# Kernel optimization log

Measured on AMD Instinct MI355X. Metric: run time of the kernel, lower is better.

## Reference

```python
import jax, jax.numpy as jnp
import numpy as np
from jax import lax

B, IN_N, OUT_N, SEQ, HID = 8, 16, 16, 256, 64
NUM_C = 64 + 3  # grid_size + spline_order
EPS_LN = 1e-5


def setup_inputs():
    key = jax.random.key(0)
    k = jax.random.split(key, 8)
    f32 = jnp.float32
    return {
        "x_in": jax.random.normal(k[0], (B, IN_N, SEQ, HID), f32),
        "proj_x_prev": jax.random.normal(k[1], (B, IN_N, SEQ, HID), f32),
        "spline_weights": jax.random.normal(k[2], (IN_N, OUT_N, NUM_C), f32) * 0.1,
        "base_scales": 0.6 + 0.1 * jax.random.normal(k[3], (IN_N, OUT_N), f32),
        "tau": jax.random.normal(k[4], (IN_N, OUT_N), f32) * 0.1 + 0.1,
        "temperature": jnp.array(1.0, f32),
        "omiga": jnp.full((IN_N, OUT_N), 0.2, f32),
        "W2": jax.random.normal(k[5], (OUT_N, HID, HID), f32) / np.sqrt(HID).astype(np.float32),
        "b_param": jnp.zeros((OUT_N, SEQ, HID), f32),
        "ln_w": jnp.ones((OUT_N, HID), f32),
        "ln_b": jnp.zeros((OUT_N, HID), f32),
        "alpha": jnp.full((OUT_N,), 0.5, f32),
        "beta": jnp.ones((OUT_N,), f32),
        "gamma": jnp.full((OUT_N,), 0.5, f32),
        "theta": jnp.ones((OUT_N,), f32),
        "conv_w": jax.random.normal(k[6], (OUT_N, HID, 1, 3, 3), f32) * 0.1,
    }


def _layernorm(x, w=None, b=None):
    mu = jnp.mean(x, -1, keepdims=True)
    var = jnp.mean((x - mu) ** 2, -1, keepdims=True)
    y = (x - mu) / jnp.sqrt(var + EPS_LN)
    if w is not None:
        y = y * w + b
    return y


def _dwconv(x, w):
    # x: [b, C, 16, 16]; w: [C, 1, 3, 3]; depthwise conv, SAME padding
    return lax.conv_general_dilated(
        x, w, (1, 1), "SAME",
        dimension_numbers=("NCHW", "OIHW", "NCHW"),
        feature_group_count=x.shape[1])


def _forward(x_in, proj_x_prev, spline_weights, base_scales, tau, temperature,
             omiga, W2, b_param, ln_w, ln_b, alpha, beta, gamma, theta, conv_w):
    b, in_n, seq, feat = x_in.shape
    num_c = spline_weights.shape[-1]
    grid = jnp.linspace(-1.0, 1.0, num_c)
    h = 2.0 / (num_c - 1)

    x_energy = jnp.mean(x_in, -1)  # [b,i,s]
    x_norm = jnp.clip(
        x_energy / (jnp.max(jnp.abs(x_energy), -1, keepdims=True) + 1e-8),
        -0.99, 0.99)

    # cubic B-spline basis (masked branches -> nested where)
    dist = jnp.abs(x_norm[..., None] - grid) / h  # [b,i,s,c]
    basis = jnp.where(dist < 1.0, 2.0 / 3.0 - dist ** 2 + dist ** 3 / 2.0,
            jnp.where(dist < 2.0, (2.0 - dist) ** 3 / 6.0, jnp.zeros_like(dist)))

    base_feat = jax.nn.silu(x_norm)[:, :, None, :] * base_scales[None, :, :, None]  # [b,i,j,s]
    spline_feat = jnp.einsum("bisc,ijc->bijs", basis, spline_weights)
    edge_resp = base_feat + spline_feat
    # [b,i,j,s,f]
    activated = (edge_resp[..., None] + jnp.abs(omiga)[None, :, :, None, None]) * x_in[:, :, None]

    t_val = jnp.abs(temperature) + 1e-4
    edge_energies = jnp.mean(jnp.abs(activated), axis=(-1, -2))  # [b,i,j]
    tau_abs = jnp.abs(tau)  # [i,j]
    mask = jax.nn.sigmoid((edge_energies - tau_abs[None]) / t_val)  # [b,i,j]

    # attention kernel W1, vectorized over output neuron j
    mid = in_n // 2
    mult = edge_energies / (tau_abs[None] + 1e-8)  # [b,i,j]
    wp = proj_x_prev[:, :, None] * (mult * mask)[..., None, None]  # [b,i,j,s,d]
    d = wp.shape[-1]
    K = jnp.transpose(wp[:, :mid], (0, 2, 3, 1, 4)).reshape(b, -1, seq, mid * d)
    Q = jnp.transpose(wp[:, mid:2 * mid], (0, 2, 3, 1, 4)).reshape(b, -1, seq, mid * d)
    K, Q = _layernorm(K), _layernorm(Q)
    raw = jnp.einsum("bjsk,bjtk->bjst", K, Q) / (jnp.sqrt(jnp.float32(mid * d)) * t_val)
    W1 = jax.nn.softmax(raw, axis=-1)  # [b,j,s,s]

    # masked mean over input neurons -> per-neuron SplineWeightLayer (vectorized)
    x = jnp.mean(activated * mask[..., None, None], axis=1)  # [b,j,s,f]
    xn = _layernorm(x, ln_w[None, :, None, :], ln_b[None, :, None, :])
    x_prime = jnp.einsum("bjsf,jfo->bjso", xn, W2) + b_param[None]  # [b,j,s,o]
    o = x_prime.shape[-1]

    # depthwise 3x3 conv on 16x16 spatial view, per-j kernels
    xsp = jnp.transpose(x_prime, (1, 0, 3, 2)).reshape(-1, b, o, 16, 16)  # [j,b,o,16,16]
    w3 = jax.vmap(_dwconv)(xsp, conv_w)  # [j,b,o,16,16]
    w3 = jnp.transpose(w3.reshape(-1, b, o, seq), (1, 0, 3, 2))  # [b,j,s,o]

    eye = jnp.eye(seq, dtype=x_prime.dtype)
    ak = (jnp.abs(beta)[None, :, None, None] * W1
          + jnp.abs(alpha)[None, :, None, None] * eye[None, None])
    glob = jnp.einsum("bjst,bjto->bjso", ak, x_prime)
    combined = glob + jnp.abs(theta)[None, :, None, None] * w3
    # residual_proj is Identity since in_hidden == out_hidden
    out = combined + gamma[None, :, None, None] * x
    return out, x_prime  # both [b, out_n, seq, out_hidden]


def reference(x_in, proj_x_prev, spline_weights, base_scales, tau, temperature,
              omiga, W2, b_param, ln_w, ln_b, alpha, beta, gamma, theta, conv_w):
    return _forward(x_in, proj_x_prev, spline_weights, base_scales, tau, temperature,
                    omiga, W2, b_param, ln_w, ln_b, alpha, beta, gamma, theta, conv_w)
```

## Files before the change

### kernel.cpp

```cpp
#include <hip/hip_runtime.h>

#define EPSLN 1e-5f

typedef short bf16x8 __attribute__((ext_vector_type(8)));
typedef float f32x4 __attribute__((ext_vector_type(4)));
typedef unsigned short u16;
typedef unsigned short u16x8 __attribute__((ext_vector_type(8)));

__device__ __forceinline__ float wsum(float v){
  #pragma unroll
  for(int o=32;o;o>>=1) v += __shfl_xor(v,o);
  return v;
}
__device__ __forceinline__ float wmax(float v){
  #pragma unroll
  for(int o=32;o;o>>=1) v = fmaxf(v,__shfl_xor(v,o));
  return v;
}
__device__ __forceinline__ u16 f2bf(float f){
  unsigned int u = __float_as_uint(f);
  u = (u + 0x7FFFu + ((u>>16)&1u)) >> 16;
  return (u16)u;
}
__device__ __forceinline__ float bf2f(u16 h){
  return __uint_as_float(((unsigned int)h)<<16);
}

__global__ void __launch_bounds__(256) kA(
                   const float* __restrict__ xin, const float* __restrict__ p,
                   const float* __restrict__ W2,
                   float* __restrict__ xe, float* __restrict__ xa,
                   float* __restrict__ Sv, float* __restrict__ SSv,
                   u16* __restrict__ xinb, u16* __restrict__ phi, u16* __restrict__ plo,
                   u16* __restrict__ w2B){
  int t = threadIdx.x;
  int rl = t>>3, q = t&7;
  int row = blockIdx.x*32 + rl;
  const float4* xr = (const float4*)(xin + row*64 + q*8);
  const float4* pr = (const float4*)(p   + row*64 + q*8);
  float s1=0.f,s2=0.f,s3=0.f,s4=0.f;
  u16x8 xb, ph, pl;
  #pragma unroll
  for(int k=0;k<2;k++){
    float4 xv = xr[k];
    float4 pv = pr[k];
    s1 += xv.x+xv.y+xv.z+xv.w;
    s2 += fabsf(xv.x)+fabsf(xv.y)+fabsf(xv.z)+fabsf(xv.w);
    s3 += pv.x+pv.y+pv.z+pv.w;
    s4 += pv.x*pv.x+pv.y*pv.y+pv.z*pv.z+pv.w*pv.w;
    int o = k*4;
    xb[o+0]=f2bf(xv.x); xb[o+1]=f2bf(xv.y); xb[o+2]=f2bf(xv.z); xb[o+3]=f2bf(xv.w);
    u16 h0=f2bf(pv.x), h1=f2bf(pv.y), h2=f2bf(pv.z), h3=f2bf(pv.w);
    ph[o+0]=h0; ph[o+1]=h1; ph[o+2]=h2; ph[o+3]=h3;
    pl[o+0]=f2bf(pv.x-bf2f(h0)); pl[o+1]=f2bf(pv.y-bf2f(h1));
    pl[o+2]=f2bf(pv.z-bf2f(h2)); pl[o+3]=f2bf(pv.w-bf2f(h3));
  }
  *(u16x8*)(xinb + row*64 + q*8) = xb;
  *(u16x8*)(phi  + row*64 + q*8) = ph;
  *(u16x8*)(plo  + row*64 + q*8) = pl;
  s1 += __shfl_xor(s1,1); s1 += __shfl_xor(s1,2); s1 += __shfl_xor(s1,4);
  s2 += __shfl_xor(s2,1); s2 += __shfl_xor(s2,2); s2 += __shfl_xor(s2,4);
  s3 += __shfl_xor(s3,1); s3 += __shfl_xor(s3,2); s3 += __shfl_xor(s3,4);
  s4 += __shfl_xor(s4,1); s4 += __shfl_xor(s4,2); s4 += __shfl_xor(s4,4);
  if(q==0){ xe[row]=s1*(1.f/64.f); xa[row]=s2*(1.f/64.f); Sv[row]=s3; SSv[row]=s4; }
  if(blockIdx.x<16){
    int j = blockIdx.x;
    for(int idx=threadIdx.x; idx<4096; idx+=256){
      int f = idx>>6, o = idx&63;
      float v = W2[j*4096 + idx];
      int ks = f>>5, kb = (f>>3)&3, i = f&7;
      int nt = o>>4, col = o&15;
      int ln = kb*16 + col;
      w2B[((j*2+ks)*4 + nt)*512 + ln*8 + i] = f2bf(v);
    }
  }
}

__global__ void __launch_bounds__(256) kBE(
                   const float* __restrict__ xe, const float* __restrict__ sw,
                   const float* __restrict__ bs, const float* __restrict__ om,
                   const float* __restrict__ xa, const float* __restrict__ tau,
                   const float* __restrict__ temp,
                   u16* __restrict__ er2b, float* __restrict__ mask,
                   float* __restrict__ cc,
                   const u16* __restrict__ phi, const u16* __restrict__ plo,
                   float* __restrict__ G){
  __shared__ __align__(16) unsigned char shm[32768];
  int tid = threadIdx.x;
  if(blockIdx.x < 128){
    float* swL = (float*)shm;
    float* bsL = swL + 1072;
    float* omL = bsL + 16;
    float* red = omL + 16;
    float* redE= red + 4;
    int bi = blockIdx.x;
    int i = bi & 15;
    int w = tid>>6, lane = tid&63;
    for(int k=tid;k<16*67;k+=256) swL[k] = sw[i*16*67 + k];
    if(tid<16){ bsL[tid]=bs[i*16+tid]; omL[tid]=fabsf(om[i*16+tid]); }
    float v = xe[bi*256+tid];
    float m = wmax(fabsf(v));
    if(lane==0) red[w]=m;
    __syncthreads();
    m = fmaxf(fmaxf(red[0],red[1]),fmaxf(red[2],red[3]));
    float xn = v/(m+1e-8f);
    xn = fminf(fmaxf(xn,-0.99f),0.99f);
    float sil = xn/(1.f+expf(-xn));
    float vv = (xn+1.f)*33.f;
    int c0 = (int)floorf(vv)-1;
    float acc[16];
    #pragma unroll
    for(int j=0;j<16;j++) acc[j]=0.f;
    #pragma unroll
    for(int k=0;k<4;k++){
      int c = c0+k;
      if(c<0||c>66) continue;
      float d = fabsf(vv-(float)c);
      float bas = d<1.f ? (2.f/3.f - d*d + d*d*d*0.5f)
                : (d<2.f ? (2.f-d)*(2.f-d)*(2.f-d)*(1.f/6.f) : 0.f);
      #pragma unroll
      for(int j=0;j<16;j++) acc[j] += bas*swL[j*67+c];
    }
    float xav = xa[bi*256+tid];
    #pragma unroll
    for(int j=0;j<16;j++){
      float ev = sil*bsL[j] + acc[j] + omL[j];
      er2b[(bi*16+j)*256+tid] = f2bf(ev);
      float pe = wsum(fabsf(ev)*xav);
      if(lane==0) redE[j*4+w]=pe;
    }
    __syncthreads();
    if(tid<16){
      float e = (redE[tid*4+0]+redE[tid*4+1]+redE[tid*4+2]+redE[tid*4+3])*(1.f/256.f);
      float tv = fabsf(temp[0])+1e-4f;
      float ta = fabsf(tau[i*16+tid]);
      float mk = 1.f/(1.f+expf(-(e-ta)/tv));
      mask[bi*16+tid]=mk;
      cc[bi*16+tid]= e/(ta+1e-8f)*mk;
    }
  } else {
    u16* AfB = (u16*)shm;
    u16* BfB = AfB + 8192;
    int e = blockIdx.x - 128;
    int b = e&7, m = (e>>3)&7, sx = (e>>6)&3, ty = e>>8;
    int bm = b*8+m;
    int s0 = sx*64, t0 = ty*64;
    int row = tid>>2, dseg = tid&3;
    size_t offA = ((size_t)(b*16+m  )*256 + s0 + row)*64 + dseg*16;
    size_t offB = ((size_t)(b*16+m+8)*256 + t0 + row)*64 + dseg*16;
    int d0 = dseg*16;
    int ks0 = d0>>5, kb0 = (d0>>3)&3;
    int ks1 = (d0+8)>>5, kb1 = ((d0+8)>>3)&3;
    int lr = row&15, stile = row>>4;
    #define AOFF(h,stl,ks,ln) (((((h)*4+(stl))*2+(ks))*64 + (ln))*8)
    {
      uint4 v0 = *(const uint4*)(phi + offA);
      uint4 v1 = *(const uint4*)(phi + offA + 8);
      *(uint4*)(AfB + AOFF(0,stile,ks0,kb0*16+lr)) = v0;
      *(uint4*)(AfB + AOFF(0,stile,ks1,kb1*16+lr)) = v1;
      uint4 w0 = *(const uint4*)(plo + offA);
      uint4 w1 = *(const uint4*)(plo + offA + 8);
      *(uint4*)(AfB + AOFF(1,stile,ks0,kb0*16+lr)) = w0;
      *(uint4*)(AfB + AOFF(1,stile,ks1,kb1*16+lr)) = w1;
      uint4 x0 = *(const uint4*)(phi + offB);
      uint4 x1 = *(const uint4*)(phi + offB + 8);
      *(uint4*)(BfB + AOFF(0,stile,ks0,kb0*16+lr)) = x0;
      *(uint4*)(BfB + AOFF(0,stile,ks1,kb1*16+lr)) = x1;
      uint4 y0 = *(const uint4*)(plo + offB);
      uint4 y1 = *(const uint4*)(plo + offB + 8);
      *(uint4*)(BfB + AOFF(1,stile,ks0,kb0*16+lr)) = y0;
      *(uint4*)(BfB + AOFF(1,stile,ks1,kb1*16+lr)) = y1;
    }
    __syncthreads();
    int w = tid>>6, lane = tid&63;
    bf16x8 ah0 = *(const bf16x8*)(AfB + AOFF(0,w,0,lane));
    bf16x8 ah1 = *(const bf16x8*)(AfB + AOFF(0,w,1,lane));
    bf16x8 al0 = *(const bf16x8*)(AfB + AOFF(1,w,0,lane));
    bf16x8 al1 = *(const bf16x8*)(AfB + AOFF(1,w,1,lane));
    f32x4 acc[4];
    #pragma unroll
    for(int tt=0;tt<4;tt++) acc[tt] = (f32x4){0.f,0.f,0.f,0.f};
    #pragma unroll
    for(int tt=0;tt<4;tt++){
      bf16x8 bh0 = *(const bf16x8*)(BfB + AOFF(0,tt,0,lane));
      bf16x8 bh1 = *(const bf16x8*)(BfB + AOFF(0,tt,1,lane));
      bf16x8 bl0 = *(const bf16x8*)(BfB + AOFF(1,tt,0,lane));
      bf16x8 bl1 = *(const bf16x8*)(BfB + AOFF(1,tt,1,lane));
      acc[tt] = __builtin_amdgcn_mfma_f32_16x16x32_bf16(ah0, bh0, acc[tt], 0,0,0);
      acc[tt] = __builtin_amdgcn_mfma_f32_16x16x32_bf16(ah1, bh1, acc[tt], 0,0,0);
      acc[tt] = __builtin_amdgcn_mfma_f32_16x16x32_bf16(ah0, bl0, acc[tt], 0,0,0);
      acc[tt] = __builtin_amdgcn_mfma_f32_16x16x32_bf16(ah1, bl1, acc[tt], 0,0,0);
      acc[tt] = __builtin_amdgcn_mfma_f32_16x16x32_bf16(al0, bh0, acc[tt], 0,0,0);
      acc[tt] = __builtin_amdgcn_mfma_f32_16x16x32_bf16(al1, bh1, acc[tt], 0,0,0);
    }
    int col = lane&15, r4 = lane>>4;
    #pragma unroll
    for(int tt=0;tt<4;tt++){
      #pragma unroll
      for(int r=0;r<4;r++){
        G[((size_t)bm*256 + s0 + w*16 + r4*4 + r)*256 + t0 + tt*16 + col] = acc[tt][r];
      }
    }
    #undef AOFF
  }
}

__global__ void __launch_bounds__(256) kD(
                   const u16* __restrict__ xinb, const u16* __restrict__ er2b,
                   const float* __restrict__ mask, const u16* __restrict__ w2B,
                   const float* __restrict__ lnw, const float* __restrict__ lnb,
                   const float* __restrict__ bp,
                   u16* __restrict__ xoutb, float* __restrict__ xp,
                   u16* __restrict__ xpB,
                   const float* __restrict__ Sv, const float* __restrict__ SSv,
                   const float* __restrict__ cc,
                   float* __restrict__ mKv, float* __restrict__ rKv,
                   float* __restrict__ mQv, float* __restrict__ rQv){
  int bid = blockIdx.x;
  int tid = threadIdx.x;
  if(bid >= 2048){
    int sid = bid - 2048;
    int b = sid&7, j = sid>>3;
    int t = tid;
    float sk=0,ssk=0,sq=0,ssq=0;
    #pragma unroll
    for(int m=0;m<8;m++){
      float ck = cc[(b*16+m)*16+j];
      float cq = cc[(b*16+m+8)*16+j];
      sk  += ck*Sv[(b*16+m)*256+t];
      ssk += ck*ck*SSv[(b*16+m)*256+t];
      sq  += cq*Sv[(b*16+m+8)*256+t];
      ssq += cq*cq*SSv[(b*16+m+8)*256+t];
    }
    float mk = sk*(1.f/512.f);
    float vk = ssk*(1.f/512.f) - mk*mk;
    float mq = sq*(1.f/512.f);
    float vq = ssq*(1.f/512.f) - mq*mq;
    int o = (b*16+j)*256+t;
    mKv[o]=mk; rKv[o]=rsqrtf(vk+EPSLN);
    mQv[o]=mq; rQv[o]=rsqrtf(vq+EPSLN);
    return;
  }
  int b = bid&7, j = (bid>>3)&15, st = bid>>7;
  int w = tid>>6, lane = tid&63;
  __shared__ __align__(16) u16 xnS[16*64];
  __shared__ float mcL[16];
  if(tid<16) mcL[tid]=mask[(b*16+tid)*16+j];
  __syncthreads();
  int bj = b*16+j;
  unsigned char* xnB = (unsigned char*)xnS;
  int ss = lane>>4, fq = lane&15;
  int sl = w*4 + ss;
  int s  = st*16 + sl;
  float4 lw4 = *(const float4*)(lnw + j*64 + fq*4);
  float4 lb4 = *(const float4*)(lnb + j*64 + fq*4);
  float acc0=0.f,acc1=0.f,acc2=0.f,acc3=0.f;
  #pragma unroll
  for(int i=0;i<16;i++){
    float er = bf2f(er2b[((b*16+i)*16+j)*256+s])*mcL[i];
    ushort4 xv = *(const ushort4*)(xinb + ((size_t)(b*16+i)*256+s)*64 + fq*4);
    acc0 += er*bf2f(xv.x);
    acc1 += er*bf2f(xv.y);
    acc2 += er*bf2f(xv.z);
    acc3 += er*bf2f(xv.w);
  }
  acc0*=(1.f/16.f); acc1*=(1.f/16.f); acc2*=(1.f/16.f); acc3*=(1.f/16.f);
  {
    u16 pk[4]={f2bf(acc0),f2bf(acc1),f2bf(acc2),f2bf(acc3)};
    *(ushort4*)(xoutb + ((size_t)bj*256+s)*64 + fq*4) = *(ushort4*)pk;
  }
  float part = acc0+acc1+acc2+acc3;
  part += __shfl_xor(part,1); part += __shfl_xor(part,2);
  part += __shfl_xor(part,4); part += __shfl_xor(part,8);
  float mu = part*(1.f/64.f);
  float d0=acc0-mu, d1=acc1-mu, d2=acc2-mu, d3=acc3-mu;
  float p2 = d0*d0+d1*d1+d2*d2+d3*d3;
  p2 += __shfl_xor(p2,1); p2 += __shfl_xor(p2,2);
  p2 += __shfl_xor(p2,4); p2 += __shfl_xor(p2,8);
  float rstd = rsqrtf(p2*(1.f/64.f)+EPSLN);
  {
    u16 xn[4] = { f2bf(d0*rstd*lw4.x + lb4.x), f2bf(d1*rstd*lw4.y + lb4.y),
                  f2bf(d2*rstd*lw4.z + lb4.z), f2bf(d3*rstd*lw4.w + lb4.w) };
    *(ushort4*)(xnB + ((sl*128 + fq*8) ^ ((sl&7)<<4))) = *(ushort4*)xn;
  }
  __syncthreads();
  f32x4 acc = {0.f,0.f,0.f,0.f};
  int m = lane&15, kb = lane>>4;
  #pragma unroll
  for(int ks=0;ks<2;ks++){
    bf16x8 a = *(const bf16x8*)(xnB + ((m*128 + ks*64 + kb*16) ^ ((m&7)<<4)));
    bf16x8 bfr = *(const bf16x8*)(w2B + ((j*2+ks)*4 + w)*512 + lane*8);
    acc = __builtin_amdgcn_mfma_f32_16x16x32_bf16(a, bfr, acc, 0, 0, 0);
  }
  int f = w*16 + m;
  u16 pk[4];
  #pragma unroll
  for(int r=0;r<4;r++){
    int si = kb*4 + r;
    int s2 = st*16 + si;
    float xpr = acc[r] + bp[((size_t)j*256+s2)*64+f];
    xp[((size_t)bj*256+s2)*64+f] = xpr;
    pk[r] = f2bf(xpr);
  }
  int s0 = st*16 + kb*4;
  int flat = ((s0>>5)*4 + w)*512 + ((s0>>3)&3)*128 + m*8 + (s0&7);
  *(ushort4*)(xpB + (size_t)bj*16384 + flat) = *(ushort4*)pk;
}

__global__ void __launch_bounds__(256) kF(
    const float* __restrict__ G, const float* __restrict__ cc,
    const float* __restrict__ mKv, const float* __restrict__ rKv,
    const float* __restrict__ mQv, const float* __restrict__ rQv,
    const float* __restrict__ xp, const u16* __restrict__ xpB,
    const float* __restrict__ cw,
    const u16* __restrict__ xarrb, const float* __restrict__ temp,
    const float* __restrict__ alpha, const float* __restrict__ beta,
    const float* __restrict__ gamma_, const float* __restrict__ theta,
    float* __restrict__ out){
  int b = blockIdx.x, jp = blockIdx.y, st = blockIdx.z;
  int j0 = jp*4;
  int tid = threadIdx.x, w = tid>>6, lane = tid&63;
  __shared__ __align__(16) unsigned char ovl[26112];
  unsigned char* prA = ovl;
  unsigned char* prB = ovl + 8192;
  float* xpT = (float*)ovl;
  float tv = fabsf(temp[0])+1e-4f;
  float inv = 1.f/(sqrtf(512.f)*tv);
  float aM0[8],aM1[8],aM2[8],aM3[8];
  #pragma unroll
  for(int m=0;m<8;m++){
    float4 ck = *(const float4*)(cc + (b*16+m  )*16 + j0);
    float4 cq = *(const float4*)(cc + (b*16+m+8)*16 + j0);
    aM0[m]=ck.x*cq.x; aM1[m]=ck.y*cq.y; aM2[m]=ck.z*cq.z; aM3[m]=ck.w*cq.w;
  }
  int bj0 = b*16+j0;
  float4 mQ4a = *(const float4*)(mQv + (size_t)(bj0  )*256 + lane*4);
  float4 rQ4a = *(const float4*)(rQv + (size_t)(bj0  )*256 + lane*4);
  float4 mQ4b = *(const float4*)(mQv + (size_t)(bj0+1)*256 + lane*4);
  float4 rQ4b = *(const float4*)(rQv + (size_t)(bj0+1)*256 + lane*4);
  float4 mQ4c = *(const float4*)(mQv + (size_t)(bj0+2)*256 + lane*4);
  float4 rQ4c = *(const float4*)(rQv + (size_t)(bj0+2)*256 + lane*4);
  float4 mQ4d = *(const float4*)(mQv + (size_t)(bj0+3)*256 + lane*4);
  float4 rQ4d = *(const float4*)(rQv + (size_t)(bj0+3)*256 + lane*4);
  const float* Gb = G + (size_t)(b*8)*65536;
  ushort4 pk2[4], pk3[4];
  #pragma unroll
  for(int q=0;q<4;q++){
    int si = w*4+q;
    int s = st*16 + si;
    f32x4 dt0={0.f,0.f,0.f,0.f}, dt1={0.f,0.f,0.f,0.f};
    f32x4 dt2={0.f,0.f,0.f,0.f}, dt3={0.f,0.f,0.f,0.f};
    #pragma unroll
    for(int m=0;m<8;m++){
      f32x4 g4 = *(const f32x4*)(Gb + (size_t)m*65536 + s*256 + lane*4);
      dt0 += aM0[m]*g4; dt1 += aM1[m]*g4;
      dt2 += aM2[m]*g4; dt3 += aM3[m]*g4;
    }
    #define SMK(JJ, DT, MQ, RQ, PKOUT) { \
      float mKs = 512.f*mKv[(size_t)(bj0+JJ)*256 + s], rKs = rKv[(size_t)(bj0+JJ)*256 + s]; \
      float e0 = __expf((DT[0] - mKs*MQ.x)*rKs*RQ.x*inv); \
      float e1 = __expf((DT[1] - mKs*MQ.y)*rKs*RQ.y*inv); \
      float e2 = __expf((DT[2] - mKs*MQ.z)*rKs*RQ.z*inv); \
      float e3 = __expf((DT[3] - mKs*MQ.w)*rKs*RQ.w*inv); \
      float isf = 1.f/wsum(e0+e1+e2+e3); \
      u16 pk[4] = {f2bf(e0*isf), f2bf(e1*isf), f2bf(e2*isf), f2bf(e3*isf)}; \
      PKOUT = *(ushort4*)pk; }
    ushort4 t0v, t1v;
    SMK(0, dt0, mQ4a, rQ4a, t0v)
    SMK(1, dt1, mQ4b, rQ4b, t1v)
    int poff = (si*512 + lane*8) ^ ((si&7)<<4);
    *(ushort4*)(prA + poff) = t0v;
    *(ushort4*)(prB + poff) = t1v;
    SMK(2, dt2, mQ4c, rQ4c, pk2[q])
    SMK(3, dt3, mQ4d, rQ4d, pk3[q])
    #undef SMK
  }
  __syncthreads();
  int m_ = lane&15, kb = lane>>4;
  f32x4 av0={0.f,0.f,0.f,0.f}, av1={0.f,0.f,0.f,0.f};
  f32x4 av2={0.f,0.f,0.f,0.f}, av3={0.f,0.f,0.f,0.f};
  const u16* xpB0 = xpB + (size_t)(bj0  )*16384;
  const u16* xpB1 = xpB + (size_t)(bj0+1)*16384;
  const u16* xpB2 = xpB + (size_t)(bj0+2)*16384;
  const u16* xpB3 = xpB + (size_t)(bj0+3)*16384;
  #pragma unroll
  for(int ks=0;ks<8;ks++){
    int aoff = (m_*512 + ks*64 + kb*16) ^ ((m_&7)<<4);
    int boff = ((ks*4 + w)*64 + lane)*8;
    bf16x8 a0 = *(const bf16x8*)(prA + aoff);
    bf16x8 a1 = *(const bf16x8*)(prB + aoff);
    av0 = __builtin_amdgcn_mfma_f32_16x16x32_bf16(a0, *(const bf16x8*)(xpB0 + boff), av0, 0,0,0);
    av1 = __builtin_amdgcn_mfma_f32_16x16x32_bf16(a1, *(const bf16x8*)(xpB1 + boff), av1, 0,0,0);
  }
  __syncthreads();
  #pragma unroll
  for(int q=0;q<4;q++){
    int si = w*4+q;
    int poff = (si*512 + lane*8) ^ ((si&7)<<4);
    *(ushort4*)(prA + poff) = pk2[q];
    *(ushort4*)(prB + poff) = pk3[q];
  }
  __syncthreads();
  #pragma unroll
  for(int ks=0;ks<8;ks++){
    int aoff = (m_*512 + ks*64 + kb*16) ^ ((m_&7)<<4);
    int boff = ((ks*4 + w)*64 + lane)*8;
    bf16x8 a2 = *(const bf16x8*)(prA + aoff);
    bf16x8 a3 = *(const bf16x8*)(prB + aoff);
    av2 = __builtin_amdgcn_mfma_f32_16x16x32_bf16(a2, *(const bf16x8*)(xpB2 + boff), av2, 0,0,0);
    av3 = __builtin_amdgcn_mfma_f32_16x16x32_bf16(a3, *(const bf16x8*)(xpB3 + boff), av3, 0,0,0);
  }
  int f = w*16 + m_;
  #pragma unroll
  for(int pass=0; pass<2; pass++){
    __syncthreads();
    for(int idx4 = tid; idx4 < 1536; idx4 += 256){
      int jj = idx4 / 768;
      int rem = idx4 - jj*768;
      int rr_i = rem >> 8;
      int pos = rem & 255;
      int ci = pos>>4, f4 = pos&15;
      int grow = st - 1 + rr_i;
      float4 v = {0.f,0.f,0.f,0.f};
      if(grow>=0 && grow<16){
        v = *(const float4*)(xp + ((size_t)(b*16+j0+pass*2+jj)*256 + grow*16 + ci)*64 + f4*4);
      }
      *(float4*)(xpT + ((jj*3+rr_i)*16+ci)*68 + f4*4) = v;
    }
    __syncthreads();
    #pragma unroll
    for(int jj=0;jj<2;jj++){
      int j = j0 + pass*2 + jj;
      int bj = b*16+j;
      f32x4 acc = pass==0 ? (jj?av1:av0) : (jj?av3:av2);
      float al = fabsf(alpha[j]), be=fabsf(beta[j]), th=fabsf(theta[j]), ga=gamma_[j];
      const float* wq = cw + (j*64+f)*9;
      float w0=wq[0],w1=wq[1],w2=wq[2],w3v=wq[3],w4=wq[4],w5=wq[5],w6=wq[6],w7=wq[7],w8=wq[8];
      #pragma unroll
      for(int r=0;r<4;r++){
        int si = kb*4 + r;
        int s = st*16 + si;
        float gl = acc[r];
        float cv=0.f;
        #pragma unroll
        for(int dr=0;dr<3;dr++){
          float kw0 = dr==0?w0:(dr==1?w3v:w6);
          float kw1 = dr==0?w1:(dr==1?w4:w7);
          float kw2 = dr==0?w2:(dr==1?w5:w8);
          const float* rowp = xpT + ((jj*3+dr)*16)*68;
          if(si>0)  cv += rowp[(si-1)*68+f]*kw0;
                    cv += rowp[(si  )*68+f]*kw1;
          if(si<15) cv += rowp[(si+1)*68+f]*kw2;
        }
        float diag = xpT[((jj*3+1)*16+si)*68+f];
        size_t gi = ((size_t)bj*256+s)*64+f;
        out[gi] = be*gl + al*diag + th*cv + ga*bf2f(xarrb[gi]);
      }
    }
  }
}

extern "C" void kernel_launch(void* const* d_in, const int* in_sizes, int n_in,
                              void* d_out, int out_size, void* d_ws, size_t ws_size,
                              hipStream_t stream) {
  const float* xin = (const float*)d_in[0];
  const float* pxp = (const float*)d_in[1];
  const float* sw  = (const float*)d_in[2];
  const float* bs  = (const float*)d_in[3];
  const float* tau = (const float*)d_in[4];
  const float* temp= (const float*)d_in[5];
  const float* om  = (const float*)d_in[6];
  const float* W2  = (const float*)d_in[7];
  const float* bp  = (const float*)d_in[8];
  const float* lnw = (const float*)d_in[9];
  const float* lnb = (const float*)d_in[10];
  const float* alpha=(const float*)d_in[11];
  const float* beta= (const float*)d_in[12];
  const float* gam = (const float*)d_in[13];
  const float* theta=(const float*)d_in[14];
  const float* cw  = (const float*)d_in[15];
  float* outp = (float*)d_out;
  float* xpo  = outp + 2097152;

  float* ws  = (float*)d_ws;
  float* xe  = ws;
  float* xa  = xe + 32768;
  float* Sv  = xa + 32768;
  float* SSv = Sv + 32768;
  u16*   er2b= (u16*)(SSv + 32768);
  float* mask= (float*)(er2b) + 524288;
  float* ccv = mask + 2048;
  float* mKv = ccv + 2048;
  float* rKv = mKv + 32768;
  float* mQv = rKv + 32768;
  float* rQv = mQv + 32768;
  float* Gv  = rQv + 32768;
  u16* xvb = (u16*)(Gv + 4194304);
  u16* xpB = xvb + 2097152;
  u16* w2B = xpB + 2097152;
  u16* xinb= w2B + 65536;
  u16* phi = xinb + 2097152;
  u16* plo = phi + 2097152;

  kA<<<1024,256,0,stream>>>(xin,pxp,W2,xe,xa,Sv,SSv,xinb,phi,plo,w2B);
  kBE<<<1152,256,0,stream>>>(xe,sw,bs,om,xa,tau,temp,er2b,mask,ccv,phi,plo,Gv);
  kD<<<2176,256,0,stream>>>(xinb,er2b,mask,w2B,lnw,lnb,bp,xvb,xpo,xpB,
                            Sv,SSv,ccv,mKv,rKv,mQv,rQv);
  kF<<<dim3(8,4,16),256,0,stream>>>(Gv,ccv,mKv,rKv,mQv,rQv,xpo,xpB,cw,xvb,temp,
                                    alpha,beta,gam,theta,outp);
}
```

Measured before the change: 54.61 us.

## Process two output nodes per kD block and transpose er2b layout

The kD kernel now computes two output nodes j per block, so each loaded x_in tile is reused for two accumulations, and the grid shrinks from 2048 to 1024 main blocks. The er2b buffer is relaid out as [b,i,s,j] so kBE writes 16 values per thread with two vector stores and kD reads both j values with one 32-bit load. The cost removed is redundant x_in reads and strided scalar er2b traffic, in exchange for more registers per thread and fewer blocks for latency hiding.

```diff
diff --git a/kernel.cpp b/kernel.cpp
--- a/kernel.cpp
+++ b/kernel.cpp
@@ -122,13 +122,16 @@
       for(int j=0;j<16;j++) acc[j] += bas*swL[j*67+c];
     }
     float xav = xa[bi*256+tid];
+    u16 evb[16];
     #pragma unroll
     for(int j=0;j<16;j++){
       float ev = sil*bsL[j] + acc[j] + omL[j];
-      er2b[(bi*16+j)*256+tid] = f2bf(ev);
+      evb[j] = f2bf(ev);
       float pe = wsum(fabsf(ev)*xav);
       if(lane==0) redE[j*4+w]=pe;
     }
+    *(u16x8*)(er2b + ((size_t)bi*256+tid)*16    ) = *(u16x8*)&evb[0];
+    *(u16x8*)(er2b + ((size_t)bi*256+tid)*16 + 8) = *(u16x8*)&evb[8];
     __syncthreads();
     if(tid<16){
       float e = (redE[tid*4+0]+redE[tid*4+1]+redE[tid*4+2]+redE[tid*4+3])*(1.f/256.f);
@@ -218,8 +221,8 @@
                    float* __restrict__ mQv, float* __restrict__ rQv){
   int bid = blockIdx.x;
   int tid = threadIdx.x;
-  if(bid >= 2048){
-    int sid = bid - 2048;
+  if(bid >= 1024){
+    int sid = bid - 1024;
     int b = sid&7, j = sid>>3;
     int t = tid;
     float sk=0,ssk=0,sq=0,ssq=0;
@@ -241,70 +244,83 @@
     mQv[o]=mq; rQv[o]=rsqrtf(vq+EPSLN);
     return;
   }
-  int b = bid&7, j = (bid>>3)&15, st = bid>>7;
+  int b = bid&7, jq = (bid>>3)&7, st = bid>>6;
+  int j0 = jq*2;
   int w = tid>>6, lane = tid&63;
-  __shared__ __align__(16) u16 xnS[16*64];
-  __shared__ float mcL[16];
-  if(tid<16) mcL[tid]=mask[(b*16+tid)*16+j];
+  __shared__ __align__(16) u16 xnS[2][16*64];
+  __shared__ float mcL[32];
+  if(tid<32) mcL[tid] = mask[(b*16+(tid>>1))*16 + j0 + (tid&1)];
   __syncthreads();
-  int bj = b*16+j;
-  unsigned char* xnB = (unsigned char*)xnS;
   int ss = lane>>4, fq = lane&15;
   int sl = w*4 + ss;
   int s  = st*16 + sl;
-  float4 lw4 = *(const float4*)(lnw + j*64 + fq*4);
-  float4 lb4 = *(const float4*)(lnb + j*64 + fq*4);
-  float acc0=0.f,acc1=0.f,acc2=0.f,acc3=0.f;
+  float a00=0.f,a01=0.f,a02=0.f,a03=0.f;
+  float a10=0.f,a11=0.f,a12=0.f,a13=0.f;
   #pragma unroll
   for(int i=0;i<16;i++){
-    float er = bf2f(er2b[((b*16+i)*16+j)*256+s])*mcL[i];
+    unsigned int epk = *(const unsigned int*)(er2b + ((size_t)((b*16+i)*256+s))*16 + j0);
+    float e0 = bf2f((u16)(epk&0xFFFFu))*mcL[i*2+0];
+    float e1 = bf2f((u16)(epk>>16))   *mcL[i*2+1];
     ushort4 xv = *(const ushort4*)(xinb + ((size_t)(b*16+i)*256+s)*64 + fq*4);
-    acc0 += er*bf2f(xv.x);
-    acc1 += er*bf2f(xv.y);
-    acc2 += er*bf2f(xv.z);
-    acc3 += er*bf2f(xv.w);
-  }
-  acc0*=(1.f/16.f); acc1*=(1.f/16.f); acc2*=(1.f/16.f); acc3*=(1.f/16.f);
-  {
-    u16 pk[4]={f2bf(acc0),f2bf(acc1),f2bf(acc2),f2bf(acc3)};
-    *(ushort4*)(xoutb + ((size_t)bj*256+s)*64 + fq*4) = *(ushort4*)pk;
-  }
-  float part = acc0+acc1+acc2+acc3;
-  part += __shfl_xor(part,1); part += __shfl_xor(part,2);
-  part += __shfl_xor(part,4); part += __shfl_xor(part,8);
-  float mu = part*(1.f/64.f);
-  float d0=acc0-mu, d1=acc1-mu, d2=acc2-mu, d3=acc3-mu;
-  float p2 = d0*d0+d1*d1+d2*d2+d3*d3;
-  p2 += __shfl_xor(p2,1); p2 += __shfl_xor(p2,2);
-  p2 += __shfl_xor(p2,4); p2 += __shfl_xor(p2,8);
-  float rstd = rsqrtf(p2*(1.f/64.f)+EPSLN);
-  {
+    float x0=bf2f(xv.x), x1=bf2f(xv.y), x2=bf2f(xv.z), x3=bf2f(xv.w);
+    a00 += e0*x0; a01 += e0*x1; a02 += e0*x2; a03 += e0*x3;
+    a10 += e1*x0; a11 += e1*x1; a12 += e1*x2; a13 += e1*x3;
+  }
+  #pragma unroll
+  for(int jj=0;jj<2;jj++){
+    int j = j0+jj;
+    int bj = b*16+j;
+    float acc0 = (jj? a10:a00)*(1.f/16.f);
+    float acc1 = (jj? a11:a01)*(1.f/16.f);
+    float acc2 = (jj? a12:a02)*(1.f/16.f);
+    float acc3 = (jj? a13:a03)*(1.f/16.f);
+    {
+      u16 pk[4]={f2bf(acc0),f2bf(acc1),f2bf(acc2),f2bf(acc3)};
+      *(ushort4*)(xoutb + ((size_t)bj*256+s)*64 + fq*4) = *(ushort4*)pk;
+    }
+    float part = acc0+acc1+acc2+acc3;
+    part += __shfl_xor(part,1); part += __shfl_xor(part,2);
+    part += __shfl_xor(part,4); part += __shfl_xor(part,8);
+    float mu = part*(1.f/64.f);
+    float d0=acc0-mu, d1=acc1-mu, d2=acc2-mu, d3=acc3-mu;
+    float p2 = d0*d0+d1*d1+d2*d2+d3*d3;
+    p2 += __shfl_xor(p2,1); p2 += __shfl_xor(p2,2);
+    p2 += __shfl_xor(p2,4); p2 += __shfl_xor(p2,8);
+    float rstd = rsqrtf(p2*(1.f/64.f)+EPSLN);
+    float4 lw4 = *(const float4*)(lnw + j*64 + fq*4);
+    float4 lb4 = *(const float4*)(lnb + j*64 + fq*4);
     u16 xn[4] = { f2bf(d0*rstd*lw4.x + lb4.x), f2bf(d1*rstd*lw4.y + lb4.y),
                   f2bf(d2*rstd*lw4.z + lb4.z), f2bf(d3*rstd*lw4.w + lb4.w) };
-    *(ushort4*)(xnB + ((sl*128 + fq*8) ^ ((sl&7)<<4))) = *(ushort4*)xn;
+    *(ushort4*)((unsigned char*)&xnS[jj][0] + ((sl*128 + fq*8) ^ ((sl&7)<<4))) = *(ushort4*)xn;
   }
   __syncthreads();
-  f32x4 acc = {0.f,0.f,0.f,0.f};
   int m = lane&15, kb = lane>>4;
   #pragma unroll
-  for(int ks=0;ks<2;ks++){
-    bf16x8 a = *(const bf16x8*)(xnB + ((m*128 + ks*64 + kb*16) ^ ((m&7)<<4)));
-    bf16x8 bfr = *(const bf16x8*)(w2B + ((j*2+ks)*4 + w)*512 + lane*8);
-    acc = __builtin_amdgcn_mfma_f32_16x16x32_bf16(a, bfr, acc, 0, 0, 0);
-  }
-  int f = w*16 + m;
-  u16 pk[4];
-  #pragma unroll
-  for(int r=0;r<4;r++){
-    int si = kb*4 + r;
-    int s2 = st*16 + si;
-    float xpr = acc[r] + bp[((size_t)j*256+s2)*64+f];
-    xp[((size_t)bj*256+s2)*64+f] = xpr;
-    pk[r] = f2bf(xpr);
-  }
-  int s0 = st*16 + kb*4;
-  int flat = ((s0>>5)*4 + w)*512 + ((s0>>3)&3)*128 + m*8 + (s0&7);
-  *(ushort4*)(xpB + (size_t)bj*16384 + flat) = *(ushort4*)pk;
+  for(int jj=0;jj<2;jj++){
+    int j = j0+jj;
+    int bj = b*16+j;
+    f32x4 acc = {0.f,0.f,0.f,0.f};
+    unsigned char* xnB = (unsigned char*)&xnS[jj][0];
+    #pragma unroll
+    for(int ks=0;ks<2;ks++){
+      bf16x8 a = *(const bf16x8*)(xnB + ((m*128 + ks*64 + kb*16) ^ ((m&7)<<4)));
+      bf16x8 bfr = *(const bf16x8*)(w2B + ((j*2+ks)*4 + w)*512 + lane*8);
+      acc = __builtin_amdgcn_mfma_f32_16x16x32_bf16(a, bfr, acc, 0, 0, 0);
+    }
+    int f = w*16 + m;
+    u16 pk[4];
+    #pragma unroll
+    for(int r=0;r<4;r++){
+      int si = kb*4 + r;
+      int s2 = st*16 + si;
+      float xpr = acc[r] + bp[((size_t)j*256+s2)*64+f];
+      xp[((size_t)bj*256+s2)*64+f] = xpr;
+      pk[r] = f2bf(xpr);
+    }
+    int s0 = st*16 + kb*4;
+    int flat = ((s0>>5)*4 + w)*512 + ((s0>>3)&3)*128 + m*8 + (s0&7);
+    *(ushort4*)(xpB + (size_t)bj*16384 + flat) = *(ushort4*)pk;
+  }
 }
 
 __global__ void __launch_bounds__(256) kF(
@@ -504,7 +520,7 @@
 
   kA<<<1024,256,0,stream>>>(xin,pxp,W2,xe,xa,Sv,SSv,xinb,phi,plo,w2B);
   kBE<<<1152,256,0,stream>>>(xe,sw,bs,om,xa,tau,temp,er2b,mask,ccv,phi,plo,Gv);
-  kD<<<2176,256,0,stream>>>(xinb,er2b,mask,w2B,lnw,lnb,bp,xvb,xpo,xpB,
+  kD<<<1152,256,0,stream>>>(xinb,er2b,mask,w2B,lnw,lnb,bp,xvb,xpo,xpB,
                             Sv,SSv,ccv,mKv,rKv,mQv,rQv);
   kF<<<dim3(8,4,16),256,0,stream>>>(Gv,ccv,mKv,rKv,mQv,rQv,xpo,xpB,cw,xvb,temp,
                                     alpha,beta,gam,theta,outp);
```

New measurement: 52.66 us. 3.6% less time.
